# Performance work log

Hardware: AMD Instinct MI355X
Metric: run time of the kernel (lower is better)

Reference implementation:

```python
import jax, jax.numpy as jnp
import numpy as np

SEQ_LEN = 2048
BATCH = 64
INPUT_SIZE = 512
HIDDEN_SIZE = 512


def setup_inputs() -> dict:
    key = jax.random.key(0)
    k_x, k_wih, k_whh, k_bih, k_bhh = jax.random.split(key, 5)
    # PyTorch RNN init: U(-1/sqrt(hidden), 1/sqrt(hidden))
    bound = 1.0 / np.sqrt(HIDDEN_SIZE)
    inputs = jax.random.normal(k_x, (SEQ_LEN, BATCH, INPUT_SIZE), dtype=jnp.float32)
    W_ih = jax.random.uniform(k_wih, (HIDDEN_SIZE, INPUT_SIZE), minval=-bound, maxval=bound, dtype=jnp.float32)
    W_hh = jax.random.uniform(k_whh, (HIDDEN_SIZE, HIDDEN_SIZE), minval=-bound, maxval=bound, dtype=jnp.float32)
    b_ih = jax.random.uniform(k_bih, (HIDDEN_SIZE,), minval=-bound, maxval=bound, dtype=jnp.float32)
    b_hh = jax.random.uniform(k_bhh, (HIDDEN_SIZE,), minval=-bound, maxval=bound, dtype=jnp.float32)
    return {"inputs": inputs, "W_ih": W_ih, "W_hh": W_hh, "b_ih": b_ih, "b_hh": b_hh}


def reference(inputs, W_ih, W_hh, b_ih, b_hh):
    # h_t = tanh(x_t W_ih^T + b_ih + h_{t-1} W_hh^T + b_hh)
    # Precompute the input projection for all timesteps in one big GEMM.
    x_proj = jnp.einsum('sbi,hi->sbh', inputs, W_ih) + b_ih + b_hh  # [S, B, H]
    h0 = jnp.zeros((inputs.shape[1], W_hh.shape[0]), dtype=inputs.dtype)

    def step(h, xp):
        h_new = jnp.tanh(xp + h @ W_hh.T)
        return h_new, h_new

    _, out = jax.lax.scan(step, h0, x_proj)  # out: [S, B, H]
    return out.reshape(-1, W_hh.shape[0])  # [S*B, H]
```

## Files before the change

kernel.cpp:

```cpp
#include <hip/hip_runtime.h>
#include <hip/hip_bf16.h>

#define SEQ   2048
#define NBATCH 64
#define HID   512
#define KDIM  512

typedef float f32x4  __attribute__((ext_vector_type(4)));
typedef short bf16x8 __attribute__((ext_vector_type(8)));

__device__ __forceinline__ unsigned short f2bf(float f) {
  union { float f; unsigned int u; } v; v.f = f;
  unsigned int r = v.u + 0x7FFFu + ((v.u >> 16) & 1u);
  return (unsigned short)(r >> 16);
}

__device__ __forceinline__ f32x4 mfma16(bf16x8 a, bf16x8 b, f32x4 c) {
  return __builtin_amdgcn_mfma_f32_16x16x32_bf16(a, b, c, 0, 0, 0);
}

__global__ void prep_wfrag(const float* __restrict__ W, unsigned short* __restrict__ dst) {
  int tid = blockIdx.x * blockDim.x + threadIdx.x;
  int e   = tid & 7;
  int l   = (tid >> 3) & 63;
  int cfg = (tid >> 9) & 31;
  int kf  = tid >> 14;
  int n = cfg * 16 + (l & 15);
  int k = kf * 32 + (l >> 4) * 8 + e;
  dst[tid] = f2bf(W[n * KDIM + k]);
}

__global__ void prep_bsum(const float* __restrict__ a, const float* __restrict__ b,
                          float* __restrict__ out) {
  int j = threadIdx.x;
  if (j < HID) out[j] = a[j] + b[j];
}

__global__ __launch_bounds__(512) void rnn_xproj(
    const float* __restrict__ X,
    const uint4* __restrict__ BW,
    const float* __restrict__ bsum,
    float* __restrict__ out) {
  const int tid = threadIdx.x, w = tid >> 6, l = tid & 63;
  const int g = l >> 4, lr = l & 15;
  const int rowbase = blockIdx.x * 64 + (w >> 2) * 32;
  const int colw = (w & 3) * 128;

  f32x4 acc[2][8];
  #pragma unroll
  for (int cf = 0; cf < 8; ++cf) {
    float bv = bsum[colw + cf * 16 + lr];
    f32x4 z = {bv, bv, bv, bv};
    acc[0][cf] = z; acc[1][cf] = z;
  }

  #pragma unroll 1
  for (int kc = 0; kc < 16; ++kc) {
    const int kb = kc * 32 + g * 8;
    bf16x8 afr[2];
    #pragma unroll
    for (int ai = 0; ai < 2; ++ai) {
      const float* src = X + (size_t)(rowbase + ai * 16 + lr) * KDIM + kb;
      float4 lo = *reinterpret_cast<const float4*>(src);
      float4 hi = *reinterpret_cast<const float4*>(src + 4);
      bf16x8 a;
      a[0] = (short)f2bf(lo.x); a[1] = (short)f2bf(lo.y);
      a[2] = (short)f2bf(lo.z); a[3] = (short)f2bf(lo.w);
      a[4] = (short)f2bf(hi.x); a[5] = (short)f2bf(hi.y);
      a[6] = (short)f2bf(hi.z); a[7] = (short)f2bf(hi.w);
      afr[ai] = a;
    }
    #pragma unroll
    for (int cf = 0; cf < 8; ++cf) {
      const int cfg = (w & 3) * 8 + cf;
      uint4 braw = BW[(kc * 32 + cfg) * 64 + l];
      bf16x8 b = __builtin_bit_cast(bf16x8, braw);
      acc[0][cf] = mfma16(afr[0], b, acc[0][cf]);
      acc[1][cf] = mfma16(afr[1], b, acc[1][cf]);
    }
  }

  #pragma unroll
  for (int ai = 0; ai < 2; ++ai) {
    #pragma unroll
    for (int cf = 0; cf < 8; ++cf) {
      const int col = colw + cf * 16 + lr;
      #pragma unroll
      for (int r = 0; r < 4; ++r) {
        const int row = rowbase + ai * 16 + g * 4 + r;
        out[(size_t)row * HID + col] = acc[ai][cf][r];
      }
    }
  }
}

__global__ __launch_bounds__(512, 2) void rnn_scan(
    const uint4* __restrict__ BW,
    float* __restrict__ xo) {
  extern __shared__ char smem[];
  const int tid = threadIdx.x, w = tid >> 6, l = tid & 63;
  const int g = l >> 4, lr = l & 15;
  const int bg = blockIdx.x;

  {
    uint4* lb = reinterpret_cast<uint4*>(smem);
    #pragma unroll
    for (int i = 0; i < 16; ++i) lb[i * 512 + tid] = BW[i * 512 + tid];
  }
  {
    float* hz = reinterpret_cast<float*>(smem + 131072);
    #pragma unroll
    for (int i = 0; i < 8; ++i) hz[i * 512 + tid] = 0.f;
  }
  bf16x8 ar[12][4];
  #pragma unroll
  for (int kf = 0; kf < 12; ++kf)
    #pragma unroll
    for (int mf = 0; mf < 4; ++mf)
      ar[kf][mf] = __builtin_bit_cast(bf16x8,
          BW[((kf + 4) * 32 + (w * 4 + mf)) * 64 + l]);
  __syncthreads();

  const int hswz = (lr & 7) << 4;
  const int bpre = lr * 1024 + g * 16;
  const int apre = (w * 4) * 1024 + l * 16;
  const int wpre = lr * 1024 + (w * 4) * 32 + g * 8;
  float* xrow0 = xo + ((size_t)bg * 16 + lr) * HID + (size_t)(w * 4) * 16 + g * 4;

  f32x4 xv[4];
  #pragma unroll
  for (int mf = 0; mf < 4; ++mf)
    xv[mf] = *reinterpret_cast<const f32x4*>(xrow0 + mf * 16);

#define SCAN_STEP(S, RD, WR)                                                      \
  {                                                                               \
    const int s = (S);                                                            \
    f32x4 acc[4];                                                                 \
    _Pragma("unroll")                                                             \
    for (int mf = 0; mf < 4; ++mf) acc[mf] = xv[mf];                              \
    {    \
      const float* xn = xrow0 + (size_t)(s + 1 < SEQ ? s + 1 : s) * (64 * HID);   \
      _Pragma("unroll")                                                           \
      for (int mf = 0; mf < 4; ++mf)                                              \
        xv[mf] = *reinterpret_cast<const f32x4*>(xn + mf * 16);                   \
    }                                                                             \
    _Pragma("unroll")                                                             \
    for (int kf = 0; kf < 4; ++kf) {                                              \
      bf16x8 hb = *reinterpret_cast<const bf16x8*>(                               \
          smem + 131072 + (RD) + ((bpre + kf * 64) ^ hswz));                      \
      const char* ab = smem + ((kf * 32) << 10) + apre;                           \
      acc[0] = mfma16(*reinterpret_cast<const bf16x8*>(ab + 0 * 1024), hb, acc[0]); \
      acc[1] = mfma16(*reinterpret_cast<const bf16x8*>(ab + 1 * 1024), hb, acc[1]); \
      acc[2] = mfma16(*reinterpret_cast<const bf16x8*>(ab + 2 * 1024), hb, acc[2]); \
      acc[3] = mfma16(*reinterpret_cast<const bf16x8*>(ab + 3 * 1024), hb, acc[3]); \
    }                                                                             \
    _Pragma("unroll")                                                             \
    for (int kf = 0; kf < 12; ++kf) {                                             \
      bf16x8 hb = *reinterpret_cast<const bf16x8*>(                               \
          smem + 131072 + (RD) + ((bpre + (kf + 4) * 64) ^ hswz));                \
      acc[0] = mfma16(ar[kf][0], hb, acc[0]);                                     \
      acc[1] = mfma16(ar[kf][1], hb, acc[1]);                                     \
      acc[2] = mfma16(ar[kf][2], hb, acc[2]);                                     \
      acc[3] = mfma16(ar[kf][3], hb, acc[3]);                                     \
    }                                                                             \
                     \
    float* orow = xrow0 + (size_t)s * (64 * HID);                                 \
    _Pragma("unroll")                                                             \
    for (int mf = 0; mf < 4; ++mf) {                                              \
      f32x4 hv;                                                                   \
      _Pragma("unroll")                                                           \
      for (int r = 0; r < 4; ++r) {                                               \
        const float pre = acc[mf][r];                                             \
        hv[r] = 1.0f - 2.0f * __builtin_amdgcn_rcpf(1.0f + __expf(2.0f * pre));   \
      }                                                                           \
      *reinterpret_cast<f32x4*>(orow + mf * 16) = hv;                             \
      uint2 hp;                                                                   \
      hp.x = (unsigned)f2bf(hv[0]) | ((unsigned)f2bf(hv[1]) << 16);               \
      hp.y = (unsigned)f2bf(hv[2]) | ((unsigned)f2bf(hv[3]) << 16);               \
      *reinterpret_cast<uint2*>(                                                  \
          smem + 131072 + (WR) + ((wpre + mf * 32) ^ hswz)) = hp;                 \
    }                                                                             \
    asm volatile("s_waitcnt lgkmcnt(0)" ::: "memory");                            \
    __builtin_amdgcn_s_barrier();                                                 \
    __builtin_amdgcn_sched_barrier(0);                                            \
  }

  #pragma unroll 1
  for (int s2 = 0; s2 < SEQ; s2 += 2) {
    SCAN_STEP(s2,     0,     16384)
    SCAN_STEP(s2 + 1, 16384, 0)
  }
#undef SCAN_STEP
}

extern "C" void kernel_launch(void* const* d_in, const int* in_sizes, int n_in,
                              void* d_out, int out_size, void* d_ws, size_t ws_size,
                              hipStream_t stream) {
  (void)in_sizes; (void)n_in; (void)out_size;
  const float* X   = (const float*)d_in[0];
  const float* Wih = (const float*)d_in[1];
  const float* Whh = (const float*)d_in[2];
  const float* bih = (const float*)d_in[3];
  const float* bhh = (const float*)d_in[4];
  float* out = (float*)d_out;

  unsigned short* wihf = (unsigned short*)d_ws;
  unsigned short* whhf = wihf + 262144;
  float* bsum = (float*)(whhf + 262144);
  if (ws_size < (size_t)(2 * 524288 + 2048)) return;

  prep_wfrag<<<1024, 256, 0, stream>>>(Wih, wihf);
  prep_wfrag<<<1024, 256, 0, stream>>>(Whh, whhf);
  prep_bsum<<<1, 512, 0, stream>>>(bih, bhh, bsum);

  rnn_xproj<<<2048, 512, 0, stream>>>(X, (const uint4*)wihf, bsum, out);

  hipFuncSetAttribute(reinterpret_cast<const void*>(rnn_scan),
                      hipFuncAttributeMaxDynamicSharedMemorySize, 163840);
  rnn_scan<<<4, 512, 163840, stream>>>((const uint4*)whhf, out);
}
```

Measured before the change: 5.939 ms.

## Store hidden state in fragment-native LDS layout and stagger wave MFMA phases

Changes the bf16 hidden-state buffer in LDS from an XOR-swizzled row layout to a layout that already matches the MFMA B-fragment order. Each lane now reads its fragment with one contiguous 16-byte load per k-slice, with no swizzle arithmetic. Odd waves run the register-held weight phase before the LDS-weight phase, and even waves do the reverse, so LDS weight reads are spread across waves instead of all waves contending at once. MFMA issue is also wrapped in s_setprio. The risk is bank conflicts on the new write pattern, or scheduling changes from the divergent per-wave code order.

```diff
diff --git a/kernel.cpp b/kernel.cpp
--- a/kernel.cpp
+++ b/kernel.cpp
@@ -121,69 +121,79 @@
           BW[((kf + 4) * 32 + (w * 4 + mf)) * 64 + l]);
   __syncthreads();
 
-  const int hswz = (lr & 7) << 4;
-  const int bpre = lr * 1024 + g * 16;
+  const int hoff = l * 16;
   const int apre = (w * 4) * 1024 + l * 16;
-  const int wpre = lr * 1024 + (w * 4) * 32 + g * 8;
+  const int hwb  = (w * 2) * 1024 + (g >> 1) * 256 + (g & 1) * 8 + lr * 16;
   float* xrow0 = xo + ((size_t)bg * 16 + lr) * HID + (size_t)(w * 4) * 16 + g * 4;
+
+#define HB(kf, RD) (*reinterpret_cast<const bf16x8*>(                            \
+    smem + 131072 + (RD) + (kf) * 1024 + hoff))
+
+#define LDS_PHASE(RD)                                                            \
+  _Pragma("unroll")                                                              \
+  for (int kf = 0; kf < 4; ++kf) {                                               \
+    bf16x8 hb = HB(kf, RD);                                                      \
+    const char* ab = smem + kf * 32768 + apre;                                   \
+    __builtin_amdgcn_s_setprio(1);                                               \
+    acc[0] = mfma16(*reinterpret_cast<const bf16x8*>(ab       ), hb, acc[0]);    \
+    acc[1] = mfma16(*reinterpret_cast<const bf16x8*>(ab + 1024), hb, acc[1]);    \
+    acc[2] = mfma16(*reinterpret_cast<const bf16x8*>(ab + 2048), hb, acc[2]);    \
+    acc[3] = mfma16(*reinterpret_cast<const bf16x8*>(ab + 3072), hb, acc[3]);    \
+    __builtin_amdgcn_s_setprio(0);                                               \
+  }
+
+#define REG_PHASE(RD)                                                            \
+  _Pragma("unroll")                                                              \
+  for (int kf = 0; kf < 12; ++kf) {                                              \
+    bf16x8 hb = HB(kf + 4, RD);                                                  \
+    __builtin_amdgcn_s_setprio(1);                                               \
+    acc[0] = mfma16(ar[kf][0], hb, acc[0]);                                      \
+    acc[1] = mfma16(ar[kf][1], hb, acc[1]);                                      \
+    acc[2] = mfma16(ar[kf][2], hb, acc[2]);                                      \
+    acc[3] = mfma16(ar[kf][3], hb, acc[3]);                                      \
+    __builtin_amdgcn_s_setprio(0);                                               \
+  }
+
+#define SCAN_STEP(S, RD, WR)                                                     \
+  {                                                                              \
+    const int s = (S);                                                           \
+    f32x4 acc[4];                                                                \
+    _Pragma("unroll")                                                            \
+    for (int mf = 0; mf < 4; ++mf) acc[mf] = xv[mf];                             \
+    {         \
+      const float* xn = xrow0 + (size_t)(s + 1 < SEQ ? s + 1 : s) * (64 * HID);  \
+      _Pragma("unroll")                                                          \
+      for (int mf = 0; mf < 4; ++mf)                                             \
+        xv[mf] = *reinterpret_cast<const f32x4*>(xn + mf * 16);                  \
+    }                                                                            \
+    if (w & 1) { REG_PHASE(RD) LDS_PHASE(RD) }                                   \
+    else       { LDS_PHASE(RD) REG_PHASE(RD) }                                   \
+         \
+    float* orow = xrow0 + (size_t)s * (64 * HID);                                \
+    _Pragma("unroll")                                                            \
+    for (int mf = 0; mf < 4; ++mf) {                                             \
+      f32x4 hv;                                                                  \
+      _Pragma("unroll")                                                          \
+      for (int r = 0; r < 4; ++r) {                                              \
+        const float pre = acc[mf][r];                                            \
+        hv[r] = 1.0f - 2.0f * __builtin_amdgcn_rcpf(1.0f + __expf(2.0f * pre));  \
+      }                                                                          \
+      *reinterpret_cast<f32x4*>(orow + mf * 16) = hv;                            \
+      uint2 hp;                                                                  \
+      hp.x = (unsigned)f2bf(hv[0]) | ((unsigned)f2bf(hv[1]) << 16);              \
+      hp.y = (unsigned)f2bf(hv[2]) | ((unsigned)f2bf(hv[3]) << 16);              \
+      *reinterpret_cast<uint2*>(smem + 131072 + (WR) + hwb +                     \
+          (mf >> 1) * 1024 + (mf & 1) * 512) = hp;                               \
+    }                                                                            \
+    asm volatile("s_waitcnt lgkmcnt(0)" ::: "memory");                           \
+    __builtin_amdgcn_s_barrier();                                                \
+    __builtin_amdgcn_sched_barrier(0);                                           \
+  }
 
   f32x4 xv[4];
   #pragma unroll
   for (int mf = 0; mf < 4; ++mf)
     xv[mf] = *reinterpret_cast<const f32x4*>(xrow0 + mf * 16);
-
-#define SCAN_STEP(S, RD, WR)                                                      \
-  {                                                                               \
-    const int s = (S);                                                            \
-    f32x4 acc[4];                                                                 \
-    _Pragma("unroll")                                                             \
-    for (int mf = 0; mf < 4; ++mf) acc[mf] = xv[mf];                              \
-    {    \
-      const float* xn = xrow0 + (size_t)(s + 1 < SEQ ? s + 1 : s) * (64 * HID);   \
-      _Pragma("unroll")                                                           \
-      for (int mf = 0; mf < 4; ++mf)                                              \
-        xv[mf] = *reinterpret_cast<const f32x4*>(xn + mf * 16);                   \
-    }                                                                             \
-    _Pragma("unroll")                                                             \
-    for (int kf = 0; kf < 4; ++kf) {                                              \
-      bf16x8 hb = *reinterpret_cast<const bf16x8*>(                               \
-          smem + 131072 + (RD) + ((bpre + kf * 64) ^ hswz));                      \
-      const char* ab = smem + ((kf * 32) << 10) + apre;                           \
-      acc[0] = mfma16(*reinterpret_cast<const bf16x8*>(ab + 0 * 1024), hb, acc[0]); \
-      acc[1] = mfma16(*reinterpret_cast<const bf16x8*>(ab + 1 * 1024), hb, acc[1]); \
-      acc[2] = mfma16(*reinterpret_cast<const bf16x8*>(ab + 2 * 1024), hb, acc[2]); \
-      acc[3] = mfma16(*reinterpret_cast<const bf16x8*>(ab + 3 * 1024), hb, acc[3]); \
-    }                                                                             \
-    _Pragma("unroll")                                                             \
-    for (int kf = 0; kf < 12; ++kf) {                                             \
-      bf16x8 hb = *reinterpret_cast<const bf16x8*>(                               \
-          smem + 131072 + (RD) + ((bpre + (kf + 4) * 64) ^ hswz));                \
-      acc[0] = mfma16(ar[kf][0], hb, acc[0]);                                     \
-      acc[1] = mfma16(ar[kf][1], hb, acc[1]);                                     \
-      acc[2] = mfma16(ar[kf][2], hb, acc[2]);                                     \
-      acc[3] = mfma16(ar[kf][3], hb, acc[3]);                                     \
-    }                                                                             \
-                     \
-    float* orow = xrow0 + (size_t)s * (64 * HID);                                 \
-    _Pragma("unroll")                                                             \
-    for (int mf = 0; mf < 4; ++mf) {                                              \
-      f32x4 hv;                                                                   \
-      _Pragma("unroll")                                                           \
-      for (int r = 0; r < 4; ++r) {                                               \
-        const float pre = acc[mf][r];                                             \
-        hv[r] = 1.0f - 2.0f * __builtin_amdgcn_rcpf(1.0f + __expf(2.0f * pre));   \
-      }                                                                           \
-      *reinterpret_cast<f32x4*>(orow + mf * 16) = hv;                             \
-      uint2 hp;                                                                   \
-      hp.x = (unsigned)f2bf(hv[0]) | ((unsigned)f2bf(hv[1]) << 16);               \
-      hp.y = (unsigned)f2bf(hv[2]) | ((unsigned)f2bf(hv[3]) << 16);               \
-      *reinterpret_cast<uint2*>(                                                  \
-          smem + 131072 + (WR) + ((wpre + mf * 32) ^ hswz)) = hp;                 \
-    }                                                                             \
-    asm volatile("s_waitcnt lgkmcnt(0)" ::: "memory");                            \
-    __builtin_amdgcn_s_barrier();                                                 \
-    __builtin_amdgcn_sched_barrier(0);                                            \
-  }
 
   #pragma unroll 1
   for (int s2 = 0; s2 < SEQ; s2 += 2) {
@@ -191,6 +201,9 @@
     SCAN_STEP(s2 + 1, 16384, 0)
   }
 #undef SCAN_STEP
+#undef LDS_PHASE
+#undef REG_PHASE
+#undef HB
 }
 
 extern "C" void kernel_launch(void* const* d_in, const int* in_sizes, int n_in,
```

After: 6.756 ms. +13.8%, slower.

## Store hidden state in MFMA fragment order and prefetch first weight fragments

Applied to the files above, without the earlier changes.

Changes the LDS layout of the bf16 hidden-state double buffer so each lane reads its B fragment with a contiguous, unswizzled address (kf*1024 + lane*16), and each lane's writes scatter into that fragment order. It also preloads the kf=0 A fragments from LDS before the barrier, so the first MFMAs of the next step don't wait on LDS, and merges the waitcnt and barrier into one asm statement. The aim is to cut address arithmetic and LDS latency on the serial per-step critical path. The trade-offs are possible bank conflicts on the new write pattern and the loss of the sched_barrier.

```diff
diff --git a/kernel.cpp b/kernel.cpp
--- a/kernel.cpp
+++ b/kernel.cpp
@@ -108,7 +108,7 @@
     for (int i = 0; i < 16; ++i) lb[i * 512 + tid] = BW[i * 512 + tid];
   }
   {
-    float* hz = reinterpret_cast<float*>(smem + 131072);
+    float* hz = reinterpret_cast<float*>(smem + 147456);
     #pragma unroll
     for (int i = 0; i < 8; ++i) hz[i * 512 + tid] = 0.f;
   }
@@ -121,16 +121,21 @@
           BW[((kf + 4) * 32 + (w * 4 + mf)) * 64 + l]);
   __syncthreads();
 
-  const int hswz = (lr & 7) << 4;
-  const int bpre = lr * 1024 + g * 16;
+  const int hoff = l * 16;
   const int apre = (w * 4) * 1024 + l * 16;
-  const int wpre = lr * 1024 + (w * 4) * 32 + g * 8;
+  const int hwb  = (w * 2) * 1024 + (g >> 1) * 256 + (g & 1) * 8 + lr * 16;
   float* xrow0 = xo + ((size_t)bg * 16 + lr) * HID + (size_t)(w * 4) * 16 + g * 4;
+
+#define HB(kf, RD) (*reinterpret_cast<const bf16x8*>(                            \
+    smem + 131072 + (RD) + (kf) * 1024 + hoff))
+#define AF(kf, mf) (*reinterpret_cast<const bf16x8*>(                            \
+    smem + (kf) * 32768 + apre + (mf) * 1024))
 
   f32x4 xv[4];
   #pragma unroll
   for (int mf = 0; mf < 4; ++mf)
     xv[mf] = *reinterpret_cast<const f32x4*>(xrow0 + mf * 16);
+  bf16x8 pa0 = AF(0, 0), pa1 = AF(0, 1), pa2 = AF(0, 2), pa3 = AF(0, 3);
 
 #define SCAN_STEP(S, RD, WR)                                                      \
   {                                                                               \
@@ -138,32 +143,40 @@
     f32x4 acc[4];                                                                 \
     _Pragma("unroll")                                                             \
     for (int mf = 0; mf < 4; ++mf) acc[mf] = xv[mf];                              \
-    {    \
+    {          \
       const float* xn = xrow0 + (size_t)(s + 1 < SEQ ? s + 1 : s) * (64 * HID);   \
       _Pragma("unroll")                                                           \
       for (int mf = 0; mf < 4; ++mf)                                              \
         xv[mf] = *reinterpret_cast<const f32x4*>(xn + mf * 16);                   \
     }                                                                             \
-    _Pragma("unroll")                                                             \
-    for (int kf = 0; kf < 4; ++kf) {                                              \
-      bf16x8 hb = *reinterpret_cast<const bf16x8*>(                               \
-          smem + 131072 + (RD) + ((bpre + kf * 64) ^ hswz));                      \
-      const char* ab = smem + ((kf * 32) << 10) + apre;                           \
-      acc[0] = mfma16(*reinterpret_cast<const bf16x8*>(ab + 0 * 1024), hb, acc[0]); \
-      acc[1] = mfma16(*reinterpret_cast<const bf16x8*>(ab + 1 * 1024), hb, acc[1]); \
-      acc[2] = mfma16(*reinterpret_cast<const bf16x8*>(ab + 2 * 1024), hb, acc[2]); \
-      acc[3] = mfma16(*reinterpret_cast<const bf16x8*>(ab + 3 * 1024), hb, acc[3]); \
-    }                                                                             \
+              \
+    {                                                                             \
+      bf16x8 hb = HB(0, RD);                                                      \
+      acc[0] = mfma16(pa0, hb, acc[0]);                                           \
+      acc[1] = mfma16(pa1, hb, acc[1]);                                           \
+      acc[2] = mfma16(pa2, hb, acc[2]);                                           \
+      acc[3] = mfma16(pa3, hb, acc[3]);                                           \
+    }                                                                             \
+                                                                \
+    _Pragma("unroll")                                                             \
+    for (int kf = 1; kf < 4; ++kf) {                                              \
+      bf16x8 hb = HB(kf, RD);                                                     \
+      const char* ab = smem + kf * 32768 + apre;                                  \
+      acc[0] = mfma16(*reinterpret_cast<const bf16x8*>(ab       ), hb, acc[0]);   \
+      acc[1] = mfma16(*reinterpret_cast<const bf16x8*>(ab + 1024), hb, acc[1]);   \
+      acc[2] = mfma16(*reinterpret_cast<const bf16x8*>(ab + 2048), hb, acc[2]);   \
+      acc[3] = mfma16(*reinterpret_cast<const bf16x8*>(ab + 3072), hb, acc[3]);   \
+    }                                                                             \
+                                                               \
     _Pragma("unroll")                                                             \
     for (int kf = 0; kf < 12; ++kf) {                                             \
-      bf16x8 hb = *reinterpret_cast<const bf16x8*>(                               \
-          smem + 131072 + (RD) + ((bpre + (kf + 4) * 64) ^ hswz));                \
+      bf16x8 hb = HB(kf + 4, RD);                                                 \
       acc[0] = mfma16(ar[kf][0], hb, acc[0]);                                     \
       acc[1] = mfma16(ar[kf][1], hb, acc[1]);                                     \
       acc[2] = mfma16(ar[kf][2], hb, acc[2]);                                     \
       acc[3] = mfma16(ar[kf][3], hb, acc[3]);                                     \
     }                                                                             \
-                     \
+          \
     float* orow = xrow0 + (size_t)s * (64 * HID);                                 \
     _Pragma("unroll")                                                             \
     for (int mf = 0; mf < 4; ++mf) {                                              \
@@ -177,20 +190,23 @@
       uint2 hp;                                                                   \
       hp.x = (unsigned)f2bf(hv[0]) | ((unsigned)f2bf(hv[1]) << 16);               \
       hp.y = (unsigned)f2bf(hv[2]) | ((unsigned)f2bf(hv[3]) << 16);               \
-      *reinterpret_cast<uint2*>(                                                  \
-          smem + 131072 + (WR) + ((wpre + mf * 32) ^ hswz)) = hp;                 \
-    }                                                                             \
-    asm volatile("s_waitcnt lgkmcnt(0)" ::: "memory");                            \
-    __builtin_amdgcn_s_barrier();                                                 \
-    __builtin_amdgcn_sched_barrier(0);                                            \
+      *reinterpret_cast<uint2*>(smem + 131072 + (WR) + hwb +                      \
+          (mf >> 1) * 1024 + (mf & 1) * 512) = hp;                                \
+    }                                                                             \
+       \
+                        \
+    pa0 = AF(0, 0); pa1 = AF(0, 1); pa2 = AF(0, 2); pa3 = AF(0, 3);               \
+    asm volatile("s_waitcnt lgkmcnt(0)\n\ts_barrier" ::: "memory");               \
   }
 
   #pragma unroll 1
   for (int s2 = 0; s2 < SEQ; s2 += 2) {
-    SCAN_STEP(s2,     0,     16384)
-    SCAN_STEP(s2 + 1, 16384, 0)
+    SCAN_STEP(s2,     16384, 0)
+    SCAN_STEP(s2 + 1, 0,     16384)
   }
 #undef SCAN_STEP
+#undef HB
+#undef AF
 }
 
 extern "C" void kernel_launch(void* const* d_in, const int* in_sizes, int n_in,
```

After: 5.028 ms. 1.18x faster.
